# Performance work log

Hardware: AMD Instinct MI355X
Metric: run time of the kernel (lower is better)

Reference implementation:

```python
import jax, jax.numpy as jnp
import numpy as np


def setup_inputs() -> dict:
    key = jax.random.key(0)
    ks = jax.random.split(key, 4)
    B, C, T = 4, 256, 4096
    Cq = C // 8
    x = jax.random.normal(ks[0], (B, C, T), dtype=jnp.float32)
    Wq = jax.random.normal(ks[1], (Cq, C), dtype=jnp.float32) * (1.0 / np.sqrt(C))
    Wk = jax.random.normal(ks[2], (Cq, C), dtype=jnp.float32) * (1.0 / np.sqrt(C))
    Wv = jax.random.normal(ks[3], (C, C), dtype=jnp.float32) * (1.0 / np.sqrt(C))
    bq = jnp.zeros((Cq,), dtype=jnp.float32)
    bk = jnp.zeros((Cq,), dtype=jnp.float32)
    bv = jnp.zeros((C,), dtype=jnp.float32)
    return {"x": x, "Wq": Wq, "bq": bq, "Wk": Wk, "bk": bk, "Wv": Wv, "bv": bv}


def reference(x, Wq, bq, Wk, bk, Wv, bv):
    # x: [B, C, T]; 1x1 conv == per-timestep linear over channels
    q = jnp.einsum('oc,bct->bto', Wq, x) + bq          # [B, T, Cq]  (proj_query permuted)
    k = jnp.einsum('oc,bct->bot', Wk, x) + bk[:, None]  # [B, Cq, T]
    v = jnp.einsum('oc,bct->bot', Wv, x) + bv[:, None]  # [B, C, T]
    attn = jax.nn.softmax(jnp.einsum('bto,bos->bts', q, k), axis=-1)  # [B, T, T]
    out = jnp.einsum('bcs,bts->bct', v, attn)           # V @ attn^T
    return out + x
```

## Files before the change

### kernel.cpp

```cpp
#include <hip/hip_runtime.h>
#include <hip/hip_bf16.h>

#define BB 4
#define CC 256
#define TT 4096
#define CQ 32
#define LOG2E 1.44269504088896340736f

typedef __bf16 bf16;
typedef __bf16 bf16x4 __attribute__((ext_vector_type(4)));
typedef __bf16 bf16x8 __attribute__((ext_vector_type(8)));
typedef float floatx4 __attribute__((ext_vector_type(4)));

#define MFMA16(a, b, c) __builtin_amdgcn_mfma_f32_16x16x32_bf16(a, b, c, 0, 0, 0)

__device__ __forceinline__ void gload_lds16(const void* g, void* l) {
    __builtin_amdgcn_global_load_lds(
        (const __attribute__((address_space(1))) void*)g,
        (__attribute__((address_space(3))) void*)l, 16, 0, 0);
}

__device__ __forceinline__ void lgkm_barrier() {
    asm volatile("s_waitcnt lgkmcnt(0)" ::: "memory");
    __builtin_amdgcn_s_barrier();
    asm volatile("" ::: "memory");
}

__global__ __launch_bounds__(256) void wconv_kernel(
    const float* __restrict__ Wq, const float* __restrict__ Wk,
    const float* __restrict__ Wv, bf16* __restrict__ Wb)
{
    int i = (blockIdx.x * 256 + threadIdx.x) * 4;
    float4 v;
    if (i < 8192)       v = *(const float4*)(Wq + i);
    else if (i < 16384) v = *(const float4*)(Wk + (i - 8192));
    else                v = *(const float4*)(Wv + (i - 16384));
    bf16x4 o;
    o[0] = (bf16)v.x; o[1] = (bf16)v.y; o[2] = (bf16)v.z; o[3] = (bf16)v.w;
    *(bf16x4*)(Wb + i) = o;
}

__global__ __launch_bounds__(256) void xtproj_kernel(
    const float* __restrict__ x, const bf16* __restrict__ Wb,
    const float* __restrict__ bq, const float* __restrict__ bk,
    const float* __restrict__ bv,
    bf16* __restrict__ Qo, bf16* __restrict__ Ko, bf16* __restrict__ Vo)
{
    __shared__ float sf[64][33];
    __shared__ bf16  xbf[32][256];

    const int tid  = threadIdx.x;
    const int lane = tid & 63, w = tid >> 6;
    const int l15  = lane & 15, quad = lane >> 4;
    const int bx   = blockIdx.x, b = blockIdx.y;
    const int t0   = bx * 32;

    for (int cc = 0; cc < 4; ++cc) {
        #pragma unroll
        for (int p = 0; p < 2; ++p) {
            int cl = p * 32 + (tid >> 3);
            int t4 = (tid & 7) * 4;
            float4 v = *(const float4*)(
                x + ((size_t)(b * CC + cc * 64 + cl)) * TT + t0 + t4);
            sf[cl][t4 + 0] = v.x; sf[cl][t4 + 1] = v.y;
            sf[cl][t4 + 2] = v.z; sf[cl][t4 + 3] = v.w;
        }
        __syncthreads();
        {
            int tl = tid >> 3;
            int c8 = (tid & 7) * 8;
            bf16x8 o;
            #pragma unroll
            for (int j = 0; j < 8; ++j) o[j] = (bf16)sf[c8 + j][tl];
            int chunk = cc * 8 + ((tid & 7) ^ (tl & 7));
            *(bf16x8*)(&xbf[tl][0] + chunk * 8) = o;
        }
        __syncthreads();
    }

    const int h  = w >> 1;
    const int tl = (w & 1) * 16 + l15;
    const int t  = t0 + tl;

    const bf16* Wqb = Wb;
    const bf16* Wkb = Wb + 8192;
    const bf16* Wvb = Wb + 16384;

    const bf16* arow[10];
    if (h == 0) {
        arow[0] = Wqb + (size_t)l15 * CC;
        arow[1] = Wqb + (size_t)(16 + l15) * CC;
        arow[2] = Wkb + (size_t)l15 * CC;
        arow[3] = Wkb + (size_t)(16 + l15) * CC;
        #pragma unroll
        for (int i = 0; i < 6; ++i)
            arow[4 + i] = Wvb + (size_t)(i * 16 + l15) * CC;
    } else {
        #pragma unroll
        for (int i = 0; i < 10; ++i)
            arow[i] = Wvb + (size_t)(96 + i * 16 + l15) * CC;
    }

    floatx4 acc[10] = {};
    for (int k = 0; k < 8; ++k) {
        int chunk = (k * 4 + quad) ^ (tl & 7);
        bf16x8 xf = *(const bf16x8*)(&xbf[tl][0] + chunk * 8);
        #pragma unroll
        for (int j = 0; j < 10; ++j) {
            bf16x8 a = *(const bf16x8*)(arow[j] + k * 32 + quad * 8);
            acc[j] = MFMA16(a, xf, acc[j]);
        }
    }

    if (h == 0) {
        #pragma unroll
        for (int mt = 0; mt < 2; ++mt) {
            float4 bsq = *(const float4*)(bq + mt * 16 + quad * 4);
            float4 bsk = *(const float4*)(bk + mt * 16 + quad * 4);
            bf16x4 vq, vk;
            vq[0] = (bf16)((acc[mt][0] + bsq.x) * LOG2E);
            vq[1] = (bf16)((acc[mt][1] + bsq.y) * LOG2E);
            vq[2] = (bf16)((acc[mt][2] + bsq.z) * LOG2E);
            vq[3] = (bf16)((acc[mt][3] + bsq.w) * LOG2E);
            vk[0] = (bf16)(acc[2 + mt][0] + bsk.x);
            vk[1] = (bf16)(acc[2 + mt][1] + bsk.y);
            vk[2] = (bf16)(acc[2 + mt][2] + bsk.z);
            vk[3] = (bf16)(acc[2 + mt][3] + bsk.w);
            *(bf16x4*)(Qo + ((size_t)(b * TT + t)) * CQ + mt * 16 + quad * 4) = vq;
            *(bf16x4*)(Ko + ((size_t)(b * TT + t)) * CQ + mt * 16 + quad * 4) = vk;
        }
        #pragma unroll
        for (int vm = 0; vm < 6; ++vm) {
            float4 bs = *(const float4*)(bv + vm * 16 + quad * 4);
            #pragma unroll
            for (int r = 0; r < 4; ++r)
                Vo[((size_t)(b * CC + vm * 16 + quad * 4 + r)) * TT + t] =
                    (bf16)(acc[4 + vm][r] + ((const float*)&bs)[r]);
        }
    } else {
        #pragma unroll
        for (int i = 0; i < 10; ++i) {
            int vm = 6 + i;
            float4 bs = *(const float4*)(bv + vm * 16 + quad * 4);
            #pragma unroll
            for (int r = 0; r < 4; ++r)
                Vo[((size_t)(b * CC + vm * 16 + quad * 4 + r)) * TT + t] =
                    (bf16)(acc[i][r] + ((const float*)&bs)[r]);
        }
    }
}

__global__ __launch_bounds__(256, 2) void flash_kernel(
    const bf16* __restrict__ Q, const bf16* __restrict__ K,
    const bf16* __restrict__ V, float* __restrict__ Op, float* __restrict__ lp)
{
    __shared__ __align__(16) char Va[32768];
    __shared__ __align__(16) char Vb[32768];
    __shared__ __align__(16) char Ps[16384];

    const int tid  = threadIdx.x;
    const int t0   = blockIdx.x * 64;
    const int sp   = blockIdx.y, b = blockIdx.z;
    const int lane = tid & 63, w = tid >> 6;
    const int l15  = lane & 15, quad = lane >> 4;
    const size_t sbase = (size_t)sp * (TT / 2);

    const bf16x8 qf = *(const bf16x8*)(
        Q + ((size_t)b * TT + t0 + w * 16 + l15) * CQ + quad * 8);

    const bf16* Kb = K + ((size_t)b * TT + sbase) * CQ;

    const int vchunk = (lane & 7) ^ (lane >> 3);
    const bf16* vsrc[8];
    #pragma unroll
    for (int i = 0; i < 8; ++i) {
        int c = w * 64 + i * 8 + (lane >> 3);
        vsrc[i] = V + ((size_t)(b * CC + c)) * TT + sbase + vchunk * 8;
    }

    floatx4 acc[4][4] = {};
    float lsum[4] = {};
    const int prow = w * 16 + quad * 4;

    bf16x8 kfc[4];
    #pragma unroll
    for (int nt = 0; nt < 4; ++nt)
        kfc[nt] = *(const bf16x8*)(Kb + (size_t)(nt * 16 + l15) * CQ + quad * 8);

    #pragma unroll
    for (int i = 0; i < 8; ++i)
        gload_lds16(vsrc[i], Va + w * 8192 + i * 1024);

    #define FLASH_TILE(ST, RD, WR)                                             \
    {                                                                          \
        const unsigned pb = (unsigned)((ST) & 1) * 8192u;                      \
                                                                    \
        floatx4 sc[4];                                                         \
        _Pragma("unroll")                                                      \
        for (int nt = 0; nt < 4; ++nt) {                                       \
            floatx4 z = {};                                                    \
            sc[nt] = MFMA16(qf, kfc[nt], z);                                   \
        }                                                                      \
                                                        \
        _Pragma("unroll")                                                      \
        for (int nt = 0; nt < 4; ++nt)                                         \
            _Pragma("unroll")                                                  \
            for (int r = 0; r < 4; ++r) {                                      \
                float pv = __builtin_amdgcn_exp2f(sc[nt][r]);                  \
                lsum[r] += pv;                                                 \
                int row  = prow + r;                                           \
                int s    = nt * 16 + l15;                                      \
                int slot = (s >> 3) ^ (row & 7);                               \
                *(bf16*)(Ps + pb + row * 128 + slot * 16 + (s & 7) * 2) =      \
                    (bf16)pv;                                                  \
            }                                                                  \
                                  \
        if ((ST) + 1 < 32) {                                                   \
            _Pragma("unroll")                                                  \
            for (int i = 0; i < 8; ++i)                                        \
                gload_lds16(vsrc[i] + (size_t)((ST) + 1) * 64,                 \
                            (WR) + w * 8192 + i * 1024);                       \
            _Pragma("unroll")                                                  \
            for (int nt = 0; nt < 4; ++nt)                                     \
                kfc[nt] = *(const bf16x8*)(                                    \
                    Kb + (size_t)(((ST) + 1) * 64 + nt * 16 + l15) * CQ +      \
                    quad * 8);                                                 \
        }                                                                      \
        lgkm_barrier();               \
                                                             \
        bf16x8 pa[4][2];                                                       \
        _Pragma("unroll")                                                      \
        for (int mt = 0; mt < 4; ++mt) {                                       \
            int row = mt * 16 + l15;                                           \
            _Pragma("unroll")                                                  \
            for (int kt = 0; kt < 2; ++kt) {                                   \
                int slot = (kt * 4 + quad) ^ (row & 7);                        \
                pa[mt][kt] = *(const bf16x8*)(Ps + pb + row * 128 + slot * 16);\
            }                                                                  \
        }                                                                      \
                                              \
        __builtin_amdgcn_s_setprio(1);                                         \
        _Pragma("unroll")                                                      \
        for (int kt = 0; kt < 2; ++kt)                                         \
            _Pragma("unroll")                                                  \
            for (int ntc = 0; ntc < 4; ++ntc) {                                \
                int c    = w * 64 + ntc * 16 + l15;                            \
                int slot = (kt * 4 + quad) ^ (l15 & 7);                        \
                bf16x8 vf = *(const bf16x8*)((RD) + c * 128 + slot * 16);      \
                _Pragma("unroll")                                              \
                for (int mt = 0; mt < 4; ++mt)                                 \
                    acc[mt][ntc] = MFMA16(pa[mt][kt], vf, acc[mt][ntc]);       \
            }                                                                  \
        __builtin_amdgcn_s_setprio(0);                                         \
    }

    for (int st2 = 0; st2 < 32; st2 += 2) {
        FLASH_TILE(st2,     Va, Vb);
        FLASH_TILE(st2 + 1, Vb, Va);
    }
    #undef FLASH_TILE

    #pragma unroll
    for (int r = 0; r < 4; ++r) {
        float s = lsum[r];
        s += __shfl_xor(s, 1); s += __shfl_xor(s, 2);
        s += __shfl_xor(s, 4); s += __shfl_xor(s, 8);
        lsum[r] = s;
    }

    float* op = Op + ((size_t)((sp * BB + b) * TT + t0)) * CC;
    #pragma unroll
    for (int mt = 0; mt < 4; ++mt)
        #pragma unroll
        for (int ntc = 0; ntc < 4; ++ntc)
            #pragma unroll
            for (int r = 0; r < 4; ++r)
                op[(size_t)(mt * 16 + quad * 4 + r) * CC + w * 64 + ntc * 16 + l15] =
                    acc[mt][ntc][r];
    if (l15 == 0) {
        #pragma unroll
        for (int r = 0; r < 4; ++r)
            lp[(size_t)(sp * BB + b) * TT + t0 + w * 16 + quad * 4 + r] = lsum[r];
    }
}

__global__ __launch_bounds__(256) void combine_kernel(
    const float* __restrict__ Op, const float* __restrict__ lp,
    const float* __restrict__ x, float* __restrict__ out)
{
    __shared__ float Os[32 * 260];
    __shared__ float Ls[32];
    const int tid = threadIdx.x;
    const int t0 = blockIdx.x * 32, b = blockIdx.y;

    if (tid < 32) {
        float l = lp[(size_t)b * TT + t0 + tid] + lp[(size_t)(BB + b) * TT + t0 + tid];
        Ls[tid] = 1.f / l;
    }
    const float* p0 = Op + ((size_t)(b * TT + t0)) * CC;
    const float* p1 = Op + ((size_t)((BB + b) * TT + t0)) * CC;
    #pragma unroll
    for (int it = 0; it < 8; ++it) {
        int chunk = it * 256 + tid;
        int t = chunk >> 6, c4 = (chunk & 63) * 4;
        float4 a = *(const float4*)(p0 + (size_t)t * CC + c4);
        float4 c2 = *(const float4*)(p1 + (size_t)t * CC + c4);
        Os[t * 260 + c4 + 0] = a.x + c2.x;
        Os[t * 260 + c4 + 1] = a.y + c2.y;
        Os[t * 260 + c4 + 2] = a.z + c2.z;
        Os[t * 260 + c4 + 3] = a.w + c2.w;
    }
    __syncthreads();

    const int tq = (tid & 7) * 4, crow = tid >> 3;
    #pragma unroll
    for (int pass = 0; pass < 8; ++pass) {
        int c = pass * 32 + crow;
        size_t base = ((size_t)(b * CC + c)) * TT + t0 + tq;
        float4 xr = *(const float4*)(x + base);
        float4 o;
        o.x = Os[(tq + 0) * 260 + c] * Ls[tq + 0] + xr.x;
        o.y = Os[(tq + 1) * 260 + c] * Ls[tq + 1] + xr.y;
        o.z = Os[(tq + 2) * 260 + c] * Ls[tq + 2] + xr.z;
        o.w = Os[(tq + 3) * 260 + c] * Ls[tq + 3] + xr.w;
        *(float4*)(out + base) = o;
    }
}

extern "C" void kernel_launch(void* const* d_in, const int* in_sizes, int n_in,
                              void* d_out, int out_size, void* d_ws, size_t ws_size,
                              hipStream_t stream) {
    const float* x  = (const float*)d_in[0];
    const float* Wq = (const float*)d_in[1];
    const float* bq = (const float*)d_in[2];
    const float* Wk = (const float*)d_in[3];
    const float* bk = (const float*)d_in[4];
    const float* Wv = (const float*)d_in[5];
    const float* bv = (const float*)d_in[6];
    float* out = (float*)d_out;

    char* ws = (char*)d_ws;
    bf16*  Wb = (bf16*)ws;
    bf16*  Qw = (bf16*)(ws + 163840);
    bf16*  Kw = (bf16*)(ws + 163840 + 1048576);
    bf16*  Vw = (bf16*)(ws + 163840 + 2097152);
    char*  R  = ws + 163840 + 2097152 + 8388608;
    float* Op = (float*)R;
    float* lp = (float*)(R + 33554432);

    wconv_kernel<<<dim3(80), 256, 0, stream>>>(Wq, Wk, Wv, Wb);
    xtproj_kernel<<<dim3(128, BB), 256, 0, stream>>>(x, Wb, bq, bk, bv, Qw, Kw, Vw);
    flash_kernel<<<dim3(64, 2, BB), 256, 0, stream>>>(Qw, Kw, Vw, Op, lp);
    combine_kernel<<<dim3(128, BB), 256, 0, stream>>>(Op, lp, x, out);
}
```

Baseline: 157.9 us.

## Software-pipeline QK scores and exp one tile ahead of PV MFMAs

Restructures the flash loop so the score MFMA, exp2 and P store for tile N+1 are computed while tile N's P is consumed by the PV MFMAs. A prologue computes the first tile's P, and the per-tile barrier moves to the end of the iteration, which gives one barrier per tile placed after the PV work. The aim is to overlap the exp/VALU and LDS-write latency with matrix work and cut barrier stalls. This adds register pressure because scores and K fragments are held live across the PV phase.

```diff
diff --git a/kernel.cpp b/kernel.cpp
--- a/kernel.cpp
+++ b/kernel.cpp
@@ -186,48 +186,53 @@
     #pragma unroll
     for (int nt = 0; nt < 4; ++nt)
         kfc[nt] = *(const bf16x8*)(Kb + (size_t)(nt * 16 + l15) * CQ + quad * 8);
-
     #pragma unroll
     for (int i = 0; i < 8; ++i)
         gload_lds16(vsrc[i], Va + w * 8192 + i * 1024);
-
-    #define FLASH_TILE(ST, RD, WR)                                             \
+    {
+        floatx4 sc0[4];
+        #pragma unroll
+        for (int nt = 0; nt < 4; ++nt) {
+            floatx4 z = {};
+            sc0[nt] = MFMA16(qf, kfc[nt], z);
+        }
+        #pragma unroll
+        for (int nt = 0; nt < 4; ++nt)
+            #pragma unroll
+            for (int r = 0; r < 4; ++r) {
+                float pv = __builtin_amdgcn_exp2f(sc0[nt][r]);
+                lsum[r] += pv;
+                int row  = prow + r;
+                int s    = nt * 16 + l15;
+                int slot = (s >> 3) ^ (row & 7);
+                *(bf16*)(Ps + row * 128 + slot * 16 + (s & 7) * 2) = (bf16)pv;
+            }
+    }
+    #pragma unroll
+    for (int nt = 0; nt < 4; ++nt)
+        kfc[nt] = *(const bf16x8*)(Kb + (size_t)(64 + nt * 16 + l15) * CQ + quad * 8);
+    lgkm_barrier();
+
+    #define FLASH_TILE(N, RD, WR, PC, PN)                                      \
     {                                                                          \
-        const unsigned pb = (unsigned)((ST) & 1) * 8192u;                      \
-                                                                    \
+        const bool more = (N) + 1 < 32;                                        \
+               \
+        if (more) {                                                            \
+            _Pragma("unroll")                                                  \
+            for (int i = 0; i < 8; ++i)                                        \
+                gload_lds16(vsrc[i] + (size_t)((N) + 1) * 64,                  \
+                            (WR) + w * 8192 + i * 1024);                       \
+        }                                                                      \
+                              \
         floatx4 sc[4];                                                         \
-        _Pragma("unroll")                                                      \
-        for (int nt = 0; nt < 4; ++nt) {                                       \
-            floatx4 z = {};                                                    \
-            sc[nt] = MFMA16(qf, kfc[nt], z);                                   \
+        if (more) {                                                            \
+            _Pragma("unroll")                                                  \
+            for (int nt = 0; nt < 4; ++nt) {                                   \
+                floatx4 z = {};                                                \
+                sc[nt] = MFMA16(qf, kfc[nt], z);                               \
+            }                                                                  \
         }                                                                      \
-                                                        \
-        _Pragma("unroll")                                                      \
-        for (int nt = 0; nt < 4; ++nt)                                         \
-            _Pragma("unroll")                                                  \
-            for (int r = 0; r < 4; ++r) {                                      \
-                float pv = __builtin_amdgcn_exp2f(sc[nt][r]);                  \
-                lsum[r] += pv;                                                 \
-                int row  = prow + r;                                           \
-                int s    = nt * 16 + l15;                                      \
-                int slot = (s >> 3) ^ (row & 7);                               \
-                *(bf16*)(Ps + pb + row * 128 + slot * 16 + (s & 7) * 2) =      \
-                    (bf16)pv;                                                  \
-            }                                                                  \
-                                  \
-        if ((ST) + 1 < 32) {                                                   \
-            _Pragma("unroll")                                                  \
-            for (int i = 0; i < 8; ++i)                                        \
-                gload_lds16(vsrc[i] + (size_t)((ST) + 1) * 64,                 \
-                            (WR) + w * 8192 + i * 1024);                       \
-            _Pragma("unroll")                                                  \
-            for (int nt = 0; nt < 4; ++nt)                                     \
-                kfc[nt] = *(const bf16x8*)(                                    \
-                    Kb + (size_t)(((ST) + 1) * 64 + nt * 16 + l15) * CQ +      \
-                    quad * 8);                                                 \
-        }                                                                      \
-        lgkm_barrier();               \
-                                                             \
+         \
         bf16x8 pa[4][2];                                                       \
         _Pragma("unroll")                                                      \
         for (int mt = 0; mt < 4; ++mt) {                                       \
@@ -235,10 +240,31 @@
             _Pragma("unroll")                                                  \
             for (int kt = 0; kt < 2; ++kt) {                                   \
                 int slot = (kt * 4 + quad) ^ (row & 7);                        \
-                pa[mt][kt] = *(const bf16x8*)(Ps + pb + row * 128 + slot * 16);\
+                pa[mt][kt] = *(const bf16x8*)((PC) + row * 128 + slot * 16);   \
             }                                                                  \
         }                                                                      \
-                                              \
+             \
+        if (more) {                                                            \
+            _Pragma("unroll")                                                  \
+            for (int nt = 0; nt < 4; ++nt)                                     \
+                _Pragma("unroll")                                              \
+                for (int r = 0; r < 4; ++r) {                                  \
+                    float pv = __builtin_amdgcn_exp2f(sc[nt][r]);              \
+                    lsum[r] += pv;                                             \
+                    int row  = prow + r;                                       \
+                    int s    = nt * 16 + l15;                                  \
+                    int slot = (s >> 3) ^ (row & 7);                           \
+                    *(bf16*)((PN) + row * 128 + slot * 16 + (s & 7) * 2) =     \
+                        (bf16)pv;                                              \
+                }                                                              \
+                                \
+            const int kn = ((N) + 2 < 32) ? (N) + 2 : 31;                      \
+            _Pragma("unroll")                                                  \
+            for (int nt = 0; nt < 4; ++nt)                                     \
+                kfc[nt] = *(const bf16x8*)(                                    \
+                    Kb + (size_t)(kn * 64 + nt * 16 + l15) * CQ + quad * 8);   \
+        }                                                                      \
+               \
         __builtin_amdgcn_s_setprio(1);                                         \
         _Pragma("unroll")                                                      \
         for (int kt = 0; kt < 2; ++kt)                                         \
@@ -252,11 +278,12 @@
                     acc[mt][ntc] = MFMA16(pa[mt][kt], vf, acc[mt][ntc]);       \
             }                                                                  \
         __builtin_amdgcn_s_setprio(0);                                         \
-    }
-
-    for (int st2 = 0; st2 < 32; st2 += 2) {
-        FLASH_TILE(st2,     Va, Vb);
-        FLASH_TILE(st2 + 1, Vb, Va);
+        lgkm_barrier();             \
+    }
+
+    for (int n2 = 0; n2 < 32; n2 += 2) {
+        FLASH_TILE(n2,     Va, Vb, Ps,        Ps + 8192);
+        FLASH_TILE(n2 + 1, Vb, Va, Ps + 8192, Ps);
     }
     #undef FLASH_TILE
 
```

Measured after the change: 162.7 us. 3.0% more time.
